# Optimization experiments

Hardware: AMD Instinct MI355X
Metric: run time of the kernel (lower is better)

The kernel has to match this reference:

```python
import jax, jax.numpy as jnp
import numpy as np

E = 16        # num_experts
TOPK = 2      # num_experts_per_tok


def setup_inputs() -> dict:
    key = jax.random.key(0)
    ks = jax.random.split(key, 8)
    B, S, H, I, IS = 4, 2048, 1024, 512, 2048
    std = 0.02
    return {
        "hidden_states": jax.random.normal(ks[0], (B, S, H), jnp.float32),
        "gate_w": jax.random.normal(ks[1], (E, H), jnp.float32) * std,
        "gate_up_proj": jax.random.normal(ks[2], (E, 2 * I, H), jnp.float32) * std,
        "down_proj": jax.random.normal(ks[3], (E, H, I), jnp.float32) * std,
        "shared_gate_proj": jax.random.normal(ks[4], (IS, H), jnp.float32) * std,
        "shared_up_proj": jax.random.normal(ks[5], (IS, H), jnp.float32) * std,
        "shared_down_proj": jax.random.normal(ks[6], (H, IS), jnp.float32) * std,
        "shared_expert_gate_w": jax.random.normal(ks[7], (1, H), jnp.float32) * std,
    }


def _moe(x, gate_w, gate_up_proj, down_proj, sgp, sup, sdp, segw):
    # x: [N, H] flattened tokens
    N = x.shape[0]
    router_logits = x @ gate_w.T                      # [N, E]
    probs = jax.nn.softmax(router_logits, axis=-1)
    routing_weights, selected = jax.lax.top_k(probs, TOPK)   # [N, TOPK]
    routing_weights = routing_weights / routing_weights.sum(-1, keepdims=True)
    # combine weights scattered into dense [N, E] (per-token per-expert gate)
    combine = jnp.zeros((N, E), x.dtype).at[jnp.arange(N)[:, None], selected].add(routing_weights)

    def body(acc, ws):
        gu_w, d_w, cw = ws                            # [2I,H], [H,I], [N]
        gu = x @ gu_w.T                               # [N, 2I]
        g, u = jnp.split(gu, 2, axis=-1)
        h = jax.nn.silu(g) * u                        # [N, I]
        return acc + cw[:, None] * (h @ d_w.T), None

    expert_out, _ = jax.lax.scan(body, jnp.zeros_like(x), (gate_up_proj, down_proj, combine.T))

    # shared expert with sigmoid token gate
    shared_h = jax.nn.silu(x @ sgp.T) * (x @ sup.T)   # [N, IS]
    shared_out = (shared_h @ sdp.T) * jax.nn.sigmoid(x @ segw.T)  # [N, H]
    out = expert_out + shared_out

    # aux (load-balancing) loss
    counts = jnp.sum(jax.nn.one_hot(selected, E, dtype=x.dtype), axis=(0, 1))  # [E]
    frac_tokens = counts / (N * TOPK)
    frac_probs = probs.sum(0) / N
    aux_loss = E * jnp.sum(frac_tokens * frac_probs)
    return out, aux_loss


def reference(hidden_states, gate_w, gate_up_proj, down_proj, shared_gate_proj, shared_up_proj, shared_down_proj, shared_expert_gate_w):
    B, S, H = hidden_states.shape
    out, aux = _moe(hidden_states.reshape(-1, H), gate_w, gate_up_proj, down_proj,
                    shared_gate_proj, shared_up_proj, shared_down_proj, shared_expert_gate_w)
    return out.reshape(B, S, H), aux
```

## Files before the change

### kernel.cpp

```cpp
#include <hip/hip_runtime.h>
#include <hip/hip_bf16.h>
#include <stdint.h>


#define N_TOK 8192
#define HDIM 1024
#define NEXP 16
#define IEXP 512
#define ISH 2048

typedef __bf16 bf16x8 __attribute__((ext_vector_type(8)));
typedef float f32x4 __attribute__((ext_vector_type(4)));

#define OFF_XBF   ((size_t)0)
#define OFF_WSG   ((size_t)16777216)
#define OFF_WSU   ((size_t)20971520)
#define OFF_WSD   ((size_t)25165824)
#define OFF_SH    ((size_t)29360128)
#define OFF_HEXP  ((size_t)62914560)
#define OFF_IDS   ((size_t)79691776)
#define OFF_META  ((size_t)80216064)
#define OFF_SIG   ((size_t)80216320)
#define OFF_LG    ((size_t)80249088)
#define OFF_SLOT  ((size_t)81297664)
#define OFF_TWAB  ((size_t)81363200)

static __device__ __forceinline__ unsigned short f2bf(float f) {
  unsigned int u = __float_as_uint(f);
  u += 0x7fffu + ((u >> 16) & 1u);
  return (unsigned short)(u >> 16);
}
static __device__ __forceinline__ int pack_bf2(float a, float b) {
  return (int)f2bf(a) | ((int)f2bf(b) << 16);
}
static __device__ __forceinline__ float bf2f(unsigned short u) {
  return __uint_as_float(((unsigned int)u) << 16);
}
static __device__ __forceinline__ void gl_lds16(const void* g, void* l) {
  __builtin_amdgcn_global_load_lds(
      (const __attribute__((address_space(1))) unsigned int*)g,
      (__attribute__((address_space(3))) unsigned int*)l, 16, 0, 0);
}

__global__ void cvt_kernel(const float* __restrict__ src,
                           unsigned short* __restrict__ dst, int n4) {
  int i = blockIdx.x * 256 + threadIdx.x;
  if (i >= n4) return;
  float4 v = ((const float4*)src)[i];
  uint2 o;
  o.x = (unsigned)pack_bf2(v.x, v.y);
  o.y = (unsigned)pack_bf2(v.z, v.w);
  ((uint2*)dst)[i] = o;
}

__global__ __launch_bounds__(256) void logits_kernel(
    const float* __restrict__ X, const float* __restrict__ GW,
    const float* __restrict__ SEGW, float* __restrict__ LG,
    unsigned short* __restrict__ XBF) {
  int wid = threadIdx.x >> 6, lane = threadIdx.x & 63;
  int tok = blockIdx.x * 4 + wid;
  const float* xr = X + (size_t)tok * HDIM;
  unsigned short* xw = XBF + (size_t)tok * HDIM;
  float xv[16];
#pragma unroll
  for (int i = 0; i < 16; i++) xv[i] = xr[lane + 64 * i];
#pragma unroll
  for (int i = 0; i < 16; i++) xw[lane + 64 * i] = f2bf(xv[i]);
  float myv = 0.f;
#pragma unroll
  for (int e = 0; e < 17; e++) {
    const float* wr = (e < 16) ? (GW + (size_t)e * HDIM) : SEGW;
    float p = 0.f;
#pragma unroll
    for (int i = 0; i < 16; i++) p += xv[i] * wr[lane + 64 * i];
#pragma unroll
    for (int off = 32; off >= 1; off >>= 1) p += __shfl_xor(p, off, 64);
    if (lane == e) myv = p;
  }
  if (lane < 17) LG[(size_t)tok * 32 + lane] = myv;
}

__global__ __launch_bounds__(256) void route_kernel(
    const float* __restrict__ LG, int* __restrict__ cnt,
    float* __restrict__ pps, int* __restrict__ ids,
    int* __restrict__ slotAB, float* __restrict__ twAB,
    float* __restrict__ sig) {
  __shared__ int lcnt[16];
  __shared__ int lbase[16];
  __shared__ float lps[16];
  int tid = threadIdx.x;
  int tok = blockIdx.x * 256 + tid;
  if (tid < 16) { lcnt[tid] = 0; lps[tid] = 0.f; }
  __syncthreads();
  const float4* row = (const float4*)(LG + (size_t)tok * 32);
  float4 v0 = row[0], v1 = row[1], v2 = row[2], v3 = row[3];
  float g16 = row[4].x;
  float lg[16] = {v0.x, v0.y, v0.z, v0.w, v1.x, v1.y, v1.z, v1.w,
                  v2.x, v2.y, v2.z, v2.w, v3.x, v3.y, v3.z, v3.w};
  float mx = lg[0];
#pragma unroll
  for (int e = 1; e < 16; e++) mx = fmaxf(mx, lg[e]);
  float pr[16], s = 0.f;
#pragma unroll
  for (int e = 0; e < 16; e++) { pr[e] = __expf(lg[e] - mx); s += pr[e]; }
  float inv_s = 1.f / s;
  float p1 = -1.f, p2 = -1.f; int i1 = 0, i2 = 0;
#pragma unroll
  for (int e = 0; e < 16; e++) {
    if (pr[e] > p1) { p2 = p1; i2 = i1; p1 = pr[e]; i1 = e; }
    else if (pr[e] > p2) { p2 = pr[e]; i2 = e; }
  }
  float wsum = p1 + p2;
  int s1 = atomicAdd(&lcnt[i1], 1);
  int s2 = atomicAdd(&lcnt[i2], 1);
#pragma unroll
  for (int e = 0; e < 16; e++) atomicAdd(&lps[e], pr[e] * inv_s);
  sig[tok] = 1.f / (1.f + __expf(-g16));
  __syncthreads();
  if (tid < 16) {
    lbase[tid] = atomicAdd(&cnt[tid], lcnt[tid]);
    atomicAdd(&pps[tid], lps[tid]);
  }
  __syncthreads();
  int sl1 = lbase[i1] + s1, sl2 = lbase[i2] + s2;
  ids[i1 * N_TOK + sl1] = tok;
  ids[i2 * N_TOK + sl2] = tok;
  slotAB[tok * 2]     = (i1 << 14) | sl1;
  slotAB[tok * 2 + 1] = (i2 << 14) | sl2;
  twAB[tok * 2]     = p1 / wsum;
  twAB[tok * 2 + 1] = p2 / wsum;
}

__global__ void offs_aux_kernel(const int* __restrict__ cnt, int* __restrict__ off,
                                const float* __restrict__ probs_sum,
                                float* __restrict__ out_aux) {
  if (threadIdx.x == 0 && blockIdx.x == 0) {
    int run = 0; float aux = 0.f;
    for (int e = 0; e < NEXP; e++) {
      off[e] = run; run += cnt[e];
      aux += ((float)cnt[e] / (float)(N_TOK * 2)) * (probs_sum[e] / (float)N_TOK);
    }
    off[16] = run;
    *out_aux = (float)NEXP * aux;
  }
}

template <int MODE>
__global__ __launch_bounds__(512, 2) void gemm8p_kernel(
    const unsigned short* __restrict__ A,
    const unsigned short* __restrict__ B1,
    const unsigned short* __restrict__ B2,
    const int* __restrict__ ids, const int* __restrict__ cnt,
    const int* __restrict__ off, unsigned short* __restrict__ Out) {
  constexpr int KD = (MODE == 2) ? IEXP : HDIM;
  constexpr int NK = KD / 64;
  extern __shared__ unsigned short lds[];

  int ne, base, e;
  if constexpr (MODE == 0) { e = 0; ne = N_TOK; base = 0; }
  else { e = blockIdx.z; ne = cnt[e]; base = off[e]; }

  const int t = threadIdx.x, lane = t & 63, w = t >> 6;
  const int fr = lane & 15, hi = lane >> 4;
  const int rq = hi * 4;
  const int Rm = (w >> 2) * 64;
  const int wn = (w & 3) * 32;
  const int srow = t >> 3;
  const int sblk = t & 7;
  const int cb = (sblk ^ (srow & 7)) * 8;
  const int s0 = ((0 + hi) ^ (fr & 7)) * 8;
  const int s1 = ((4 + hi) ^ (fr & 7)) * 8;
  const f32x4 z = {0.f, 0.f, 0.f, 0.f};

#define STG_A(buf, h, kt)                                                     \
  do {                                                                        \
    gl_lds16(apt[h][0] + (kt) * 64, &lds[(buf)*32768 + (h)*8192 + t * 8]);    \
    gl_lds16(apt[h][1] + (kt) * 64,                                           \
             &lds[(buf)*32768 + (h)*8192 + 4096 + t * 8]);                    \
  } while (0)
#define STG_B(buf, h, kt)                                                     \
  do {                                                                        \
    gl_lds16(bpt[h][0] + (kt) * 64,                                           \
             &lds[(buf)*32768 + 16384 + (h)*8192 + t * 8]);                   \
    gl_lds16(bpt[h][1] + (kt) * 64,                                           \
             &lds[(buf)*32768 + 16384 + (h)*8192 + 4096 + t * 8]);            \
  } while (0)

  for (int m0 = blockIdx.y * 256; m0 < ne; m0 += gridDim.y * 256) {
    const unsigned short* apt[2][2];
    const unsigned short* bpt[2][2];
#pragma unroll
    for (int h = 0; h < 2; h++)
#pragma unroll
      for (int l = 0; l < 2; l++) {
        int r = h * 128 + l * 64 + srow;
        int arow;
        if constexpr (MODE == 0) {
          arow = m0 + r;
        } else if constexpr (MODE == 1) {
          int slot = m0 + r;
          arow = (slot < ne) ? ids[e * N_TOK + slot] : 0;
        } else {
          int ra = base + m0 + r;
          if (ra > 16383) ra = 16383;
          arow = ra;
        }
        apt[h][l] = A + (size_t)arow * KD + cb;
        if constexpr (MODE == 0) {
          int gcol = blockIdx.x * 128 + ((r >> 5) << 4) + (r & 15);
          const unsigned short* W = (r & 16) ? B2 : B1;
          bpt[h][l] = W + (size_t)gcol * HDIM + cb;
        } else if constexpr (MODE == 1) {
          int wrow = ((r & 16) ? 512 : 0) + blockIdx.x * 128 + ((r >> 5) << 4) + (r & 15);
          bpt[h][l] = B1 + ((size_t)e * 1024 + wrow) * HDIM + cb;
        } else {
          int nrow = blockIdx.x * 256 + r;
          bpt[h][l] = B1 + ((size_t)e * HDIM + nrow) * IEXP + cb;
        }
      }

    f32x4 acc[8][4];
#pragma unroll
    for (int i = 0; i < 8; i++)
#pragma unroll
      for (int j = 0; j < 4; j++) acc[i][j] = z;

    STG_A(0, 0, 0); STG_B(0, 1, 0); STG_A(0, 1, 0); STG_B(0, 0, 0);
    if (NK > 1) {
      STG_A(1, 0, 1); STG_B(1, 1, 1);
      asm volatile("s_waitcnt vmcnt(4)" ::: "memory");
    } else {
      asm volatile("s_waitcnt vmcnt(0)" ::: "memory");
    }
    __builtin_amdgcn_s_barrier();

    for (int kt = 0; kt < NK; ++kt) {
      const int c = kt & 1, nb = c ^ 1;
      const unsigned short* Ab = &lds[c * 32768];
      const unsigned short* Bb = &lds[c * 32768 + 16384];
      bf16x8 a[4][2], b[2][2];

#pragma unroll
      for (int i = 0; i < 4; i++) {
        int ro = (Rm + i * 16 + fr) * 64;
        a[i][0] = *(const bf16x8*)&Ab[ro + s0];
        a[i][1] = *(const bf16x8*)&Ab[ro + s1];
      }
#pragma unroll
      for (int j = 0; j < 2; j++) {
        int ro = (wn + j * 16 + fr) * 64;
        b[j][0] = *(const bf16x8*)&Bb[ro + s0];
        b[j][1] = *(const bf16x8*)&Bb[ro + s1];
      }
      if (kt + 1 < NK) STG_A(nb, 1, kt + 1);
      __builtin_amdgcn_s_barrier();
      asm volatile("s_waitcnt lgkmcnt(0)" ::: "memory");
      __builtin_amdgcn_s_setprio(1);
#pragma unroll
      for (int i = 0; i < 4; i++)
#pragma unroll
        for (int j = 0; j < 2; j++) {
          acc[i][j] = __builtin_amdgcn_mfma_f32_16x16x32_bf16(a[i][0], b[j][0], acc[i][j], 0, 0, 0);
          acc[i][j] = __builtin_amdgcn_mfma_f32_16x16x32_bf16(a[i][1], b[j][1], acc[i][j], 0, 0, 0);
        }
      __builtin_amdgcn_s_setprio(0);
      __builtin_amdgcn_s_barrier();

#pragma unroll
      for (int j = 0; j < 2; j++) {
        int ro = (128 + wn + j * 16 + fr) * 64;
        b[j][0] = *(const bf16x8*)&Bb[ro + s0];
        b[j][1] = *(const bf16x8*)&Bb[ro + s1];
      }
      if (kt + 1 < NK) STG_B(nb, 0, kt + 1);
      __builtin_amdgcn_s_barrier();
      asm volatile("s_waitcnt lgkmcnt(0)" ::: "memory");
      __builtin_amdgcn_s_setprio(1);
#pragma unroll
      for (int i = 0; i < 4; i++)
#pragma unroll
        for (int j = 0; j < 2; j++) {
          acc[i][2 + j] = __builtin_amdgcn_mfma_f32_16x16x32_bf16(a[i][0], b[j][0], acc[i][2 + j], 0, 0, 0);
          acc[i][2 + j] = __builtin_amdgcn_mfma_f32_16x16x32_bf16(a[i][1], b[j][1], acc[i][2 + j], 0, 0, 0);
        }
      __builtin_amdgcn_s_setprio(0);
      __builtin_amdgcn_s_barrier();

#pragma unroll
      for (int i = 0; i < 4; i++) {
        int ro = (128 + Rm + i * 16 + fr) * 64;
        a[i][0] = *(const bf16x8*)&Ab[ro + s0];
        a[i][1] = *(const bf16x8*)&Ab[ro + s1];
      }
      if (kt + 2 < NK) STG_A(c, 0, kt + 2);
      __builtin_amdgcn_s_barrier();
      asm volatile("s_waitcnt lgkmcnt(0)" ::: "memory");
      __builtin_amdgcn_s_setprio(1);
#pragma unroll
      for (int i = 0; i < 4; i++)
#pragma unroll
        for (int j = 0; j < 2; j++) {
          acc[4 + i][2 + j] = __builtin_amdgcn_mfma_f32_16x16x32_bf16(a[i][0], b[j][0], acc[4 + i][2 + j], 0, 0, 0);
          acc[4 + i][2 + j] = __builtin_amdgcn_mfma_f32_16x16x32_bf16(a[i][1], b[j][1], acc[4 + i][2 + j], 0, 0, 0);
        }
      __builtin_amdgcn_s_setprio(0);
      __builtin_amdgcn_s_barrier();

#pragma unroll
      for (int j = 0; j < 2; j++) {
        int ro = (wn + j * 16 + fr) * 64;
        b[j][0] = *(const bf16x8*)&Bb[ro + s0];
        b[j][1] = *(const bf16x8*)&Bb[ro + s1];
      }
      if (kt + 2 < NK) STG_B(c, 1, kt + 2);
      __builtin_amdgcn_s_barrier();
      asm volatile("s_waitcnt lgkmcnt(0)" ::: "memory");
      __builtin_amdgcn_s_setprio(1);
#pragma unroll
      for (int i = 0; i < 4; i++)
#pragma unroll
        for (int j = 0; j < 2; j++) {
          acc[4 + i][j] = __builtin_amdgcn_mfma_f32_16x16x32_bf16(a[i][0], b[j][0], acc[4 + i][j], 0, 0, 0);
          acc[4 + i][j] = __builtin_amdgcn_mfma_f32_16x16x32_bf16(a[i][1], b[j][1], acc[4 + i][j], 0, 0, 0);
        }
      __builtin_amdgcn_s_setprio(0);
      if (kt + 2 < NK) asm volatile("s_waitcnt vmcnt(4)" ::: "memory");
      else             asm volatile("s_waitcnt vmcnt(0)" ::: "memory");
      __builtin_amdgcn_s_barrier();
    }

#pragma unroll
    for (int i = 0; i < 8; i++) {
      int mloc = (i >> 2) * 128 + Rm + (i & 3) * 16 + rq;
      if constexpr (MODE == 2) {
#pragma unroll
        for (int j = 0; j < 4; j++) {
          int nn = blockIdx.x * 256 + (j >> 1) * 128 + wn + (j & 1) * 16 + fr;
#pragma unroll
          for (int r = 0; r < 4; r++) {
            int slot = m0 + mloc + r;
            if (slot < ne)
              Out[(size_t)(base + slot) * HDIM + nn] = f2bf(acc[i][j][r]);
          }
        }
      } else {
#pragma unroll
        for (int p = 0; p < 2; p++) {
          int cc = blockIdx.x * 128 + p * 64 + (w & 3) * 16 + fr;
#pragma unroll
          for (int r = 0; r < 4; r++) {
            int slot = m0 + mloc + r;
            float g = acc[i][2 * p][r], u = acc[i][2 * p + 1][r];
            float hv = g / (1.f + __expf(-g)) * u;
            if constexpr (MODE == 0) {
              Out[(size_t)slot * ISH + cc] = f2bf(hv);
            } else {
              if (slot < ne)
                Out[(size_t)(base + slot) * IEXP + cc] = f2bf(hv);
            }
          }
        }
      }
    }
  }
#undef STG_A
#undef STG_B
}

__global__ __launch_bounds__(256) void shared_gemm2_kernel(
    const unsigned short* __restrict__ H, const unsigned short* __restrict__ Wd,
    const float* __restrict__ sig, float* __restrict__ Out) {
  __shared__ __align__(16) unsigned short As[128 * 32];
  __shared__ __align__(16) unsigned short Bs[128 * 32];
  int m0 = blockIdx.y * 128, n0 = blockIdx.x * 128;
  int t = threadIdx.x, lane = t & 63, w = t >> 6;
  int wm = (w & 1) * 64, wn = (w >> 1) * 64;
  int arow = t >> 2, akb = (t & 3) * 8;
  const unsigned short* apA0 = H + (size_t)(m0 + arow) * ISH + akb;
  const unsigned short* apA1 = H + (size_t)(m0 + 64 + arow) * ISH + akb;
  const unsigned short* apB0 = Wd + (size_t)(n0 + arow) * ISH + akb;
  const unsigned short* apB1 = Wd + (size_t)(n0 + 64 + arow) * ISH + akb;
  f32x4 z = {0.f, 0.f, 0.f, 0.f};
  f32x4 acc[4][4];
#pragma unroll
  for (int i = 0; i < 4; i++)
#pragma unroll
    for (int j = 0; j < 4; j++) acc[i][j] = z;
  for (int k0 = 0; k0 < ISH; k0 += 32) {
    __syncthreads();
    gl_lds16(apA0 + k0, &As[t * 8]);
    gl_lds16(apA1 + k0, &As[2048 + t * 8]);
    gl_lds16(apB0 + k0, &Bs[t * 8]);
    gl_lds16(apB1 + k0, &Bs[2048 + t * 8]);
    __syncthreads();
    int fr = lane & 15, fc = (lane >> 4) * 8;
    bf16x8 af[4], bfr[4];
#pragma unroll
    for (int i = 0; i < 4; i++) {
      af[i] = *(const bf16x8*)&As[(wm + i * 16 + fr) * 32 + fc];
      bfr[i] = *(const bf16x8*)&Bs[(wn + i * 16 + fr) * 32 + fc];
    }
#pragma unroll
    for (int i = 0; i < 4; i++)
#pragma unroll
      for (int j = 0; j < 4; j++)
        acc[i][j] = __builtin_amdgcn_mfma_f32_16x16x32_bf16(af[i], bfr[j], acc[i][j], 0, 0, 0);
  }
  int col = lane & 15, rq = (lane >> 4) * 4;
#pragma unroll
  for (int i = 0; i < 4; i++)
#pragma unroll
    for (int r = 0; r < 4; r++) {
      int mm = m0 + wm + i * 16 + rq + r;
      float sg = sig[mm];
#pragma unroll
      for (int j = 0; j < 4; j++) {
        int nn = n0 + wn + j * 16 + col;
        Out[(size_t)mm * HDIM + nn] = acc[i][j][r] * sg;
      }
    }
}

__global__ __launch_bounds__(256) void combine_kernel(
    const unsigned short* __restrict__ Eout, const int* __restrict__ slotAB,
    const float* __restrict__ twAB, const int* __restrict__ off,
    float* __restrict__ Out) {
  int tok = blockIdx.x, t = threadIdx.x;
  int sa = slotAB[tok * 2], sb = slotAB[tok * 2 + 1];
  float wa = twAB[tok * 2], wb = twAB[tok * 2 + 1];
  int ra = off[sa >> 14] + (sa & 16383);
  int rb = off[sb >> 14] + (sb & 16383);
  const ushort4 a4 = *(const ushort4*)(Eout + (size_t)ra * HDIM + t * 4);
  const ushort4 b4 = *(const ushort4*)(Eout + (size_t)rb * HDIM + t * 4);
  float* po = Out + (size_t)tok * HDIM + t * 4;
  float4 o = *(const float4*)po;
  o.x += wa * bf2f(a4.x) + wb * bf2f(b4.x);
  o.y += wa * bf2f(a4.y) + wb * bf2f(b4.y);
  o.z += wa * bf2f(a4.z) + wb * bf2f(b4.z);
  o.w += wa * bf2f(a4.w) + wb * bf2f(b4.w);
  *(float4*)po = o;
}

extern "C" void kernel_launch(void* const* d_in, const int* in_sizes, int n_in,
                              void* d_out, int out_size, void* d_ws, size_t ws_size,
                              hipStream_t stream) {
  const float* X   = (const float*)d_in[0];
  const float* GW  = (const float*)d_in[1];
  const float* WGU = (const float*)d_in[2];
  const float* WDN = (const float*)d_in[3];
  const float* WSG = (const float*)d_in[4];
  const float* WSU = (const float*)d_in[5];
  const float* WSD = (const float*)d_in[6];
  const float* SEGW = (const float*)d_in[7];
  float* Out = (float*)d_out;
  char* ws = (char*)d_ws;

  unsigned short* xbf  = (unsigned short*)(ws + OFF_XBF);
  unsigned short* wsg  = (unsigned short*)(ws + OFF_WSG);
  unsigned short* wsu  = (unsigned short*)(ws + OFF_WSU);
  unsigned short* wsd  = (unsigned short*)(ws + OFF_WSD);
  unsigned short* sh   = (unsigned short*)(ws + OFF_SH);
  unsigned short* hexp = (unsigned short*)(ws + OFF_HEXP);
  int*   ids  = (int*)(ws + OFF_IDS);
  int*   cnt  = (int*)(ws + OFF_META);
  int*   off  = (int*)(ws + OFF_META + 64);
  float* pps  = (float*)(ws + OFF_META + 144);
  float* sig  = (float*)(ws + OFF_SIG);
  float* lg   = (float*)(ws + OFF_LG);
  int*   slotAB = (int*)(ws + OFF_SLOT);
  float* twAB   = (float*)(ws + OFF_TWAB);
  unsigned short* wgu_bf = (unsigned short*)(ws + OFF_SH);
  unsigned short* wdn_bf = (unsigned short*)(ws + OFF_XBF);
  unsigned short* eout   = (unsigned short*)(ws + OFF_SH);

  (void)hipFuncSetAttribute((const void*)gemm8p_kernel<0>,
                            hipFuncAttributeMaxDynamicSharedMemorySize, 131072);
  (void)hipFuncSetAttribute((const void*)gemm8p_kernel<1>,
                            hipFuncAttributeMaxDynamicSharedMemorySize, 131072);
  (void)hipFuncSetAttribute((const void*)gemm8p_kernel<2>,
                            hipFuncAttributeMaxDynamicSharedMemorySize, 131072);

  hipMemsetAsync(ws + OFF_META, 0, 256, stream);

  {
    int n4;
    n4 = (ISH * HDIM) / 4;
    cvt_kernel<<<(n4 + 255) / 256, 256, 0, stream>>>(WSG, wsg, n4);
    cvt_kernel<<<(n4 + 255) / 256, 256, 0, stream>>>(WSU, wsu, n4);
    n4 = (HDIM * ISH) / 4;
    cvt_kernel<<<(n4 + 255) / 256, 256, 0, stream>>>(WSD, wsd, n4);
  }

  logits_kernel<<<N_TOK / 4, 256, 0, stream>>>(X, GW, SEGW, lg, xbf);
  route_kernel<<<N_TOK / 256, 256, 0, stream>>>(lg, cnt, pps, ids, slotAB, twAB, sig);
  offs_aux_kernel<<<1, 64, 0, stream>>>(cnt, off, pps, Out + (size_t)N_TOK * HDIM);

  gemm8p_kernel<0><<<dim3(ISH * 2 / 256, N_TOK / 256), 512, 131072, stream>>>(
      xbf, wsg, wsu, ids, cnt, off, sh);
  shared_gemm2_kernel<<<dim3(HDIM / 128, N_TOK / 128), 256, 0, stream>>>(sh, wsd, sig, Out);

  {
    int n4 = (NEXP * 2 * IEXP * HDIM) / 4;
    cvt_kernel<<<(n4 + 255) / 256, 256, 0, stream>>>(WGU, wgu_bf, n4);
  }
  gemm8p_kernel<1><<<dim3(IEXP * 2 / 256, 8, NEXP), 512, 131072, stream>>>(
      xbf, wgu_bf, wgu_bf, ids, cnt, off, hexp);
  {
    int n4 = (NEXP * HDIM * IEXP) / 4;
    cvt_kernel<<<(n4 + 255) / 256, 256, 0, stream>>>(WDN, wdn_bf, n4);
  }
  gemm8p_kernel<2><<<dim3(HDIM / 256, 8, NEXP), 512, 131072, stream>>>(
      hexp, wdn_bf, wdn_bf, ids, cnt, off, eout);
  combine_kernel<<<N_TOK, 256, 0, stream>>>(eout, slotAB, twAB, off, Out);
}
```

Baseline: 507.7 us.

## Merge shared down-proj with expert gate-up GEMM and fuse combine via atomics

Replaces the separate shared-expert down-projection kernel and combine kernel with a unified GEMM template. One launch covers both the routed-expert gate/up GEMM and a split-K shared down-projection, so the two run concurrently. The expert down-projection now scatters weighted results into a zeroed fp32 output with atomicAdd, which removes the bf16 intermediate and the combine pass. It also drops the per-phase lgkmcnt waits and extra barriers in the inner loop, and relocates the expert weight conversions when the workspace is large enough. In exchange it adds atomic traffic, a full output memset, and nondeterministic summation order.

```diff
diff --git a/kernel.cpp b/kernel.cpp
--- a/kernel.cpp
+++ b/kernel.cpp
@@ -25,6 +25,10 @@
 #define OFF_SLOT  ((size_t)81297664)
 #define OFF_TWAB  ((size_t)81363200)
 
+#define WGU_NEW   ((size_t)81428736)
+#define WDN_NEW   ((size_t)(WGU_NEW + 33554432))
+#define NEED_MERGED ((size_t)(WDN_NEW + 16777216))
+
 static __device__ __forceinline__ unsigned short f2bf(float f) {
   unsigned int u = __float_as_uint(f);
   u += 0x7fffu + ((u >> 16) & 1u);
@@ -33,13 +37,15 @@
 static __device__ __forceinline__ int pack_bf2(float a, float b) {
   return (int)f2bf(a) | ((int)f2bf(b) << 16);
 }
-static __device__ __forceinline__ float bf2f(unsigned short u) {
-  return __uint_as_float(((unsigned int)u) << 16);
-}
 static __device__ __forceinline__ void gl_lds16(const void* g, void* l) {
   __builtin_amdgcn_global_load_lds(
       (const __attribute__((address_space(1))) unsigned int*)g,
       (__attribute__((address_space(3))) unsigned int*)l, 16, 0, 0);
+}
+static __device__ __forceinline__ void barf() {
+  asm volatile("" ::: "memory");
+  __builtin_amdgcn_s_barrier();
+  asm volatile("" ::: "memory");
 }
 
 __global__ void cvt_kernel(const float* __restrict__ src,
@@ -145,20 +151,45 @@
   }
 }
 
-template <int MODE>
-__global__ __launch_bounds__(512, 2) void gemm8p_kernel(
-    const unsigned short* __restrict__ A,
+__global__ __launch_bounds__(256) void tws_kernel(
+    const int* __restrict__ slotAB, const float* __restrict__ twAB,
+    const int* __restrict__ off, float* __restrict__ tws) {
+  int tok = blockIdx.x * 256 + threadIdx.x;
+  int sa = slotAB[tok * 2], sb = slotAB[tok * 2 + 1];
+  tws[off[sa >> 14] + (sa & 16383)] = twAB[tok * 2];
+  tws[off[sb >> 14] + (sb & 16383)] = twAB[tok * 2 + 1];
+}
+
+template <int TMODE>
+__global__ __launch_bounds__(512, 2) void g8p_kernel(
+    const unsigned short* __restrict__ A0,
+    const unsigned short* __restrict__ A1,
     const unsigned short* __restrict__ B1,
     const unsigned short* __restrict__ B2,
+    const unsigned short* __restrict__ B3,
     const int* __restrict__ ids, const int* __restrict__ cnt,
-    const int* __restrict__ off, unsigned short* __restrict__ Out) {
-  constexpr int KD = (MODE == 2) ? IEXP : HDIM;
-  constexpr int NK = KD / 64;
+    const int* __restrict__ off, const float* __restrict__ tws,
+    const float* __restrict__ sig,
+    unsigned short* __restrict__ OBf, float* __restrict__ OF, int zoff) {
   extern __shared__ unsigned short lds[];
 
-  int ne, base, e;
-  if constexpr (MODE == 0) { e = 0; ne = N_TOK; base = 0; }
-  else { e = blockIdx.z; ne = cnt[e]; base = off[e]; }
+  int rmode, e = 0, kls = 0, mt = 0;
+  if constexpr (TMODE == 13) {
+    int z = blockIdx.z + zoff;
+    if (z < 16) { rmode = 1; e = z; }
+    else { rmode = 3; int zp = z - 16; mt = (zp >> 2) * 8 + blockIdx.y; kls = zp & 3; }
+  } else if constexpr (TMODE == 2) {
+    rmode = 2; e = blockIdx.z >> 1; kls = blockIdx.z & 1;
+  } else {
+    rmode = 0;
+  }
+
+  int ne, base = 0;
+  if (rmode == 1 || rmode == 2) { ne = cnt[e]; base = off[e]; }
+  else ne = N_TOK;
+
+  const int NK = (TMODE == 0) ? 16 : (TMODE == 2) ? 4 : (rmode == 1 ? 16 : 8);
+  const int kofs = (rmode == 2) ? kls * 256 : (rmode == 3) ? kls * 512 : 0;
 
   const int t = threadIdx.x, lane = t & 63, w = t >> 6;
   const int fr = lane & 15, hi = lane >> 4;
@@ -170,7 +201,11 @@
   const int cb = (sblk ^ (srow & 7)) * 8;
   const int s0 = ((0 + hi) ^ (fr & 7)) * 8;
   const int s1 = ((4 + hi) ^ (fr & 7)) * 8;
-  const f32x4 z = {0.f, 0.f, 0.f, 0.f};
+  const f32x4 z4 = {0.f, 0.f, 0.f, 0.f};
+
+  int m0start, m0end, m0step;
+  if (rmode == 3) { m0start = mt * 256; m0end = m0start + 256; m0step = 8192; }
+  else { m0start = blockIdx.y * 256; m0end = ne; m0step = (int)gridDim.y * 256; }
 
 #define STG_A(buf, h, kt)                                                     \
   do {                                                                        \
@@ -186,7 +221,7 @@
              &lds[(buf)*32768 + 16384 + (h)*8192 + 4096 + t * 8]);            \
   } while (0)
 
-  for (int m0 = blockIdx.y * 256; m0 < ne; m0 += gridDim.y * 256) {
+  for (int m0 = m0start; m0 < m0end; m0 += m0step) {
     const unsigned short* apt[2][2];
     const unsigned short* bpt[2][2];
 #pragma unroll
@@ -194,28 +229,32 @@
 #pragma unroll
       for (int l = 0; l < 2; l++) {
         int r = h * 128 + l * 64 + srow;
-        int arow;
-        if constexpr (MODE == 0) {
-          arow = m0 + r;
-        } else if constexpr (MODE == 1) {
+        if (rmode == 0) {
+          apt[h][l] = A0 + (size_t)(m0 + r) * HDIM + cb;
+        } else if (rmode == 1) {
           int slot = m0 + r;
-          arow = (slot < ne) ? ids[e * N_TOK + slot] : 0;
-        } else {
+          int arow = (slot < ne) ? ids[e * N_TOK + slot] : 0;
+          apt[h][l] = A0 + (size_t)arow * HDIM + cb;
+        } else if (rmode == 2) {
           int ra = base + m0 + r;
           if (ra > 16383) ra = 16383;
-          arow = ra;
-        }
-        apt[h][l] = A + (size_t)arow * KD + cb;
-        if constexpr (MODE == 0) {
+          apt[h][l] = A0 + (size_t)ra * IEXP + kofs + cb;
+        } else {
+          apt[h][l] = A1 + (size_t)(m0 + r) * ISH + kofs + cb;
+        }
+        if (rmode == 0) {
           int gcol = blockIdx.x * 128 + ((r >> 5) << 4) + (r & 15);
           const unsigned short* W = (r & 16) ? B2 : B1;
           bpt[h][l] = W + (size_t)gcol * HDIM + cb;
-        } else if constexpr (MODE == 1) {
+        } else if (rmode == 1) {
           int wrow = ((r & 16) ? 512 : 0) + blockIdx.x * 128 + ((r >> 5) << 4) + (r & 15);
           bpt[h][l] = B1 + ((size_t)e * 1024 + wrow) * HDIM + cb;
+        } else if (rmode == 2) {
+          int nrow = blockIdx.x * 256 + r;
+          bpt[h][l] = B1 + ((size_t)e * HDIM + nrow) * IEXP + kofs + cb;
         } else {
           int nrow = blockIdx.x * 256 + r;
-          bpt[h][l] = B1 + ((size_t)e * HDIM + nrow) * IEXP + cb;
+          bpt[h][l] = B3 + (size_t)nrow * ISH + kofs + cb;
         }
       }
 
@@ -223,16 +262,12 @@
 #pragma unroll
     for (int i = 0; i < 8; i++)
 #pragma unroll
-      for (int j = 0; j < 4; j++) acc[i][j] = z;
+      for (int j = 0; j < 4; j++) acc[i][j] = z4;
 
     STG_A(0, 0, 0); STG_B(0, 1, 0); STG_A(0, 1, 0); STG_B(0, 0, 0);
-    if (NK > 1) {
-      STG_A(1, 0, 1); STG_B(1, 1, 1);
-      asm volatile("s_waitcnt vmcnt(4)" ::: "memory");
-    } else {
-      asm volatile("s_waitcnt vmcnt(0)" ::: "memory");
-    }
-    __builtin_amdgcn_s_barrier();
+    STG_A(1, 0, 1); STG_B(1, 1, 1);
+    asm volatile("s_waitcnt vmcnt(4)" ::: "memory");
+    barf();
 
     for (int kt = 0; kt < NK; ++kt) {
       const int c = kt & 1, nb = c ^ 1;
@@ -253,8 +288,6 @@
         b[j][1] = *(const bf16x8*)&Bb[ro + s1];
       }
       if (kt + 1 < NK) STG_A(nb, 1, kt + 1);
-      __builtin_amdgcn_s_barrier();
-      asm volatile("s_waitcnt lgkmcnt(0)" ::: "memory");
       __builtin_amdgcn_s_setprio(1);
 #pragma unroll
       for (int i = 0; i < 4; i++)
@@ -264,7 +297,7 @@
           acc[i][j] = __builtin_amdgcn_mfma_f32_16x16x32_bf16(a[i][1], b[j][1], acc[i][j], 0, 0, 0);
         }
       __builtin_amdgcn_s_setprio(0);
-      __builtin_amdgcn_s_barrier();
+      barf();
 
 #pragma unroll
       for (int j = 0; j < 2; j++) {
@@ -273,8 +306,6 @@
         b[j][1] = *(const bf16x8*)&Bb[ro + s1];
       }
       if (kt + 1 < NK) STG_B(nb, 0, kt + 1);
-      __builtin_amdgcn_s_barrier();
-      asm volatile("s_waitcnt lgkmcnt(0)" ::: "memory");
       __builtin_amdgcn_s_setprio(1);
 #pragma unroll
       for (int i = 0; i < 4; i++)
@@ -284,7 +315,7 @@
           acc[i][2 + j] = __builtin_amdgcn_mfma_f32_16x16x32_bf16(a[i][1], b[j][1], acc[i][2 + j], 0, 0, 0);
         }
       __builtin_amdgcn_s_setprio(0);
-      __builtin_amdgcn_s_barrier();
+      barf();
 
 #pragma unroll
       for (int i = 0; i < 4; i++) {
@@ -293,8 +324,6 @@
         a[i][1] = *(const bf16x8*)&Ab[ro + s1];
       }
       if (kt + 2 < NK) STG_A(c, 0, kt + 2);
-      __builtin_amdgcn_s_barrier();
-      asm volatile("s_waitcnt lgkmcnt(0)" ::: "memory");
       __builtin_amdgcn_s_setprio(1);
 #pragma unroll
       for (int i = 0; i < 4; i++)
@@ -304,7 +333,7 @@
           acc[4 + i][2 + j] = __builtin_amdgcn_mfma_f32_16x16x32_bf16(a[i][1], b[j][1], acc[4 + i][2 + j], 0, 0, 0);
         }
       __builtin_amdgcn_s_setprio(0);
-      __builtin_amdgcn_s_barrier();
+      barf();
 
 #pragma unroll
       for (int j = 0; j < 2; j++) {
@@ -313,8 +342,6 @@
         b[j][1] = *(const bf16x8*)&Bb[ro + s1];
       }
       if (kt + 2 < NK) STG_B(c, 1, kt + 2);
-      __builtin_amdgcn_s_barrier();
-      asm volatile("s_waitcnt lgkmcnt(0)" ::: "memory");
       __builtin_amdgcn_s_setprio(1);
 #pragma unroll
       for (int i = 0; i < 4; i++)
@@ -326,24 +353,13 @@
       __builtin_amdgcn_s_setprio(0);
       if (kt + 2 < NK) asm volatile("s_waitcnt vmcnt(4)" ::: "memory");
       else             asm volatile("s_waitcnt vmcnt(0)" ::: "memory");
-      __builtin_amdgcn_s_barrier();
+      barf();
     }
 
 #pragma unroll
     for (int i = 0; i < 8; i++) {
       int mloc = (i >> 2) * 128 + Rm + (i & 3) * 16 + rq;
-      if constexpr (MODE == 2) {
-#pragma unroll
-        for (int j = 0; j < 4; j++) {
-          int nn = blockIdx.x * 256 + (j >> 1) * 128 + wn + (j & 1) * 16 + fr;
-#pragma unroll
-          for (int r = 0; r < 4; r++) {
-            int slot = m0 + mloc + r;
-            if (slot < ne)
-              Out[(size_t)(base + slot) * HDIM + nn] = f2bf(acc[i][j][r]);
-          }
-        }
-      } else {
+      if (rmode == 0 || rmode == 1) {
 #pragma unroll
         for (int p = 0; p < 2; p++) {
           int cc = blockIdx.x * 128 + p * 64 + (w & 3) * 16 + fr;
@@ -352,93 +368,43 @@
             int slot = m0 + mloc + r;
             float g = acc[i][2 * p][r], u = acc[i][2 * p + 1][r];
             float hv = g / (1.f + __expf(-g)) * u;
-            if constexpr (MODE == 0) {
-              Out[(size_t)slot * ISH + cc] = f2bf(hv);
-            } else {
-              if (slot < ne)
-                Out[(size_t)(base + slot) * IEXP + cc] = f2bf(hv);
+            if (rmode == 0) {
+              OBf[(size_t)slot * ISH + cc] = f2bf(hv);
+            } else if (slot < ne) {
+              OBf[(size_t)(base + slot) * IEXP + cc] = f2bf(hv);
             }
           }
         }
+      } else if (rmode == 2) {
+#pragma unroll
+        for (int r = 0; r < 4; r++) {
+          int slot = m0 + mloc + r;
+          if (slot < ne) {
+            int tok = ids[e * N_TOK + slot];
+            float tw = tws[base + slot];
+#pragma unroll
+            for (int j = 0; j < 4; j++) {
+              int nn = blockIdx.x * 256 + (j >> 1) * 128 + wn + (j & 1) * 16 + fr;
+              atomicAdd(&OF[(size_t)tok * HDIM + nn], tw * acc[i][j][r]);
+            }
+          }
+        }
+      } else {
+#pragma unroll
+        for (int r = 0; r < 4; r++) {
+          int m = m0 + mloc + r;
+          float sv = sig[m];
+#pragma unroll
+          for (int j = 0; j < 4; j++) {
+            int nn = blockIdx.x * 256 + (j >> 1) * 128 + wn + (j & 1) * 16 + fr;
+            atomicAdd(&OF[(size_t)m * HDIM + nn], sv * acc[i][j][r]);
+          }
+        }
       }
     }
   }
 #undef STG_A
 #undef STG_B
-}
-
-__global__ __launch_bounds__(256) void shared_gemm2_kernel(
-    const unsigned short* __restrict__ H, const unsigned short* __restrict__ Wd,
-    const float* __restrict__ sig, float* __restrict__ Out) {
-  __shared__ __align__(16) unsigned short As[128 * 32];
-  __shared__ __align__(16) unsigned short Bs[128 * 32];
-  int m0 = blockIdx.y * 128, n0 = blockIdx.x * 128;
-  int t = threadIdx.x, lane = t & 63, w = t >> 6;
-  int wm = (w & 1) * 64, wn = (w >> 1) * 64;
-  int arow = t >> 2, akb = (t & 3) * 8;
-  const unsigned short* apA0 = H + (size_t)(m0 + arow) * ISH + akb;
-  const unsigned short* apA1 = H + (size_t)(m0 + 64 + arow) * ISH + akb;
-  const unsigned short* apB0 = Wd + (size_t)(n0 + arow) * ISH + akb;
-  const unsigned short* apB1 = Wd + (size_t)(n0 + 64 + arow) * ISH + akb;
-  f32x4 z = {0.f, 0.f, 0.f, 0.f};
-  f32x4 acc[4][4];
-#pragma unroll
-  for (int i = 0; i < 4; i++)
-#pragma unroll
-    for (int j = 0; j < 4; j++) acc[i][j] = z;
-  for (int k0 = 0; k0 < ISH; k0 += 32) {
-    __syncthreads();
-    gl_lds16(apA0 + k0, &As[t * 8]);
-    gl_lds16(apA1 + k0, &As[2048 + t * 8]);
-    gl_lds16(apB0 + k0, &Bs[t * 8]);
-    gl_lds16(apB1 + k0, &Bs[2048 + t * 8]);
-    __syncthreads();
-    int fr = lane & 15, fc = (lane >> 4) * 8;
-    bf16x8 af[4], bfr[4];
-#pragma unroll
-    for (int i = 0; i < 4; i++) {
-      af[i] = *(const bf16x8*)&As[(wm + i * 16 + fr) * 32 + fc];
-      bfr[i] = *(const bf16x8*)&Bs[(wn + i * 16 + fr) * 32 + fc];
-    }
-#pragma unroll
-    for (int i = 0; i < 4; i++)
-#pragma unroll
-      for (int j = 0; j < 4; j++)
-        acc[i][j] = __builtin_amdgcn_mfma_f32_16x16x32_bf16(af[i], bfr[j], acc[i][j], 0, 0, 0);
-  }
-  int col = lane & 15, rq = (lane >> 4) * 4;
-#pragma unroll
-  for (int i = 0; i < 4; i++)
-#pragma unroll
-    for (int r = 0; r < 4; r++) {
-      int mm = m0 + wm + i * 16 + rq + r;
-      float sg = sig[mm];
-#pragma unroll
-      for (int j = 0; j < 4; j++) {
-        int nn = n0 + wn + j * 16 + col;
-        Out[(size_t)mm * HDIM + nn] = acc[i][j][r] * sg;
-      }
-    }
-}
-
-__global__ __launch_bounds__(256) void combine_kernel(
-    const unsigned short* __restrict__ Eout, const int* __restrict__ slotAB,
-    const float* __restrict__ twAB, const int* __restrict__ off,
-    float* __restrict__ Out) {
-  int tok = blockIdx.x, t = threadIdx.x;
-  int sa = slotAB[tok * 2], sb = slotAB[tok * 2 + 1];
-  float wa = twAB[tok * 2], wb = twAB[tok * 2 + 1];
-  int ra = off[sa >> 14] + (sa & 16383);
-  int rb = off[sb >> 14] + (sb & 16383);
-  const ushort4 a4 = *(const ushort4*)(Eout + (size_t)ra * HDIM + t * 4);
-  const ushort4 b4 = *(const ushort4*)(Eout + (size_t)rb * HDIM + t * 4);
-  float* po = Out + (size_t)tok * HDIM + t * 4;
-  float4 o = *(const float4*)po;
-  o.x += wa * bf2f(a4.x) + wb * bf2f(b4.x);
-  o.y += wa * bf2f(a4.y) + wb * bf2f(b4.y);
-  o.z += wa * bf2f(a4.z) + wb * bf2f(b4.z);
-  o.w += wa * bf2f(a4.w) + wb * bf2f(b4.w);
-  *(float4*)po = o;
 }
 
 extern "C" void kernel_launch(void* const* d_in, const int* in_sizes, int n_in,
@@ -467,20 +433,23 @@
   float* pps  = (float*)(ws + OFF_META + 144);
   float* sig  = (float*)(ws + OFF_SIG);
   float* lg   = (float*)(ws + OFF_LG);
+  float* tws  = (float*)(ws + OFF_LG);
   int*   slotAB = (int*)(ws + OFF_SLOT);
   float* twAB   = (float*)(ws + OFF_TWAB);
-  unsigned short* wgu_bf = (unsigned short*)(ws + OFF_SH);
-  unsigned short* wdn_bf = (unsigned short*)(ws + OFF_XBF);
-  unsigned short* eout   = (unsigned short*)(ws + OFF_SH);
-
-  (void)hipFuncSetAttribute((const void*)gemm8p_kernel<0>,
+
+  const bool merged = (ws_size >= NEED_MERGED);
+  unsigned short* wgu_bf = (unsigned short*)(ws + (merged ? WGU_NEW : OFF_SH));
+  unsigned short* wdn_bf = (unsigned short*)(ws + (merged ? WDN_NEW : OFF_XBF));
+
+  (void)hipFuncSetAttribute((const void*)g8p_kernel<0>,
                             hipFuncAttributeMaxDynamicSharedMemorySize, 131072);
-  (void)hipFuncSetAttribute((const void*)gemm8p_kernel<1>,
+  (void)hipFuncSetAttribute((const void*)g8p_kernel<2>,
                             hipFuncAttributeMaxDynamicSharedMemorySize, 131072);
-  (void)hipFuncSetAttribute((const void*)gemm8p_kernel<2>,
+  (void)hipFuncSetAttribute((const void*)g8p_kernel<13>,
                             hipFuncAttributeMaxDynamicSharedMemorySize, 131072);
 
   hipMemsetAsync(ws + OFF_META, 0, 256, stream);
+  hipMemsetAsync(Out, 0, (size_t)N_TOK * HDIM * 4, stream);
 
   {
     int n4;
@@ -490,26 +459,39 @@
     n4 = (HDIM * ISH) / 4;
     cvt_kernel<<<(n4 + 255) / 256, 256, 0, stream>>>(WSD, wsd, n4);
   }
+  if (merged) {
+    int n4 = (NEXP * 2 * IEXP * HDIM) / 4;
+    cvt_kernel<<<(n4 + 255) / 256, 256, 0, stream>>>(WGU, wgu_bf, n4);
+    n4 = (NEXP * HDIM * IEXP) / 4;
+    cvt_kernel<<<(n4 + 255) / 256, 256, 0, stream>>>(WDN, wdn_bf, n4);
+  }
 
   logits_kernel<<<N_TOK / 4, 256, 0, stream>>>(X, GW, SEGW, lg, xbf);
   route_kernel<<<N_TOK / 256, 256, 0, stream>>>(lg, cnt, pps, ids, slotAB, twAB, sig);
   offs_aux_kernel<<<1, 64, 0, stream>>>(cnt, off, pps, Out + (size_t)N_TOK * HDIM);
-
-  gemm8p_kernel<0><<<dim3(ISH * 2 / 256, N_TOK / 256), 512, 131072, stream>>>(
-      xbf, wsg, wsu, ids, cnt, off, sh);
-  shared_gemm2_kernel<<<dim3(HDIM / 128, N_TOK / 128), 256, 0, stream>>>(sh, wsd, sig, Out);
-
-  {
-    int n4 = (NEXP * 2 * IEXP * HDIM) / 4;
-    cvt_kernel<<<(n4 + 255) / 256, 256, 0, stream>>>(WGU, wgu_bf, n4);
-  }
-  gemm8p_kernel<1><<<dim3(IEXP * 2 / 256, 8, NEXP), 512, 131072, stream>>>(
-      xbf, wgu_bf, wgu_bf, ids, cnt, off, hexp);
-  {
-    int n4 = (NEXP * HDIM * IEXP) / 4;
-    cvt_kernel<<<(n4 + 255) / 256, 256, 0, stream>>>(WDN, wdn_bf, n4);
-  }
-  gemm8p_kernel<2><<<dim3(HDIM / 256, 8, NEXP), 512, 131072, stream>>>(
-      hexp, wdn_bf, wdn_bf, ids, cnt, off, eout);
-  combine_kernel<<<N_TOK, 256, 0, stream>>>(eout, slotAB, twAB, off, Out);
-}
+  tws_kernel<<<N_TOK / 256, 256, 0, stream>>>(slotAB, twAB, off, tws);
+
+  g8p_kernel<0><<<dim3(ISH * 2 / 256, N_TOK / 256, 1), 512, 131072, stream>>>(
+      xbf, nullptr, wsg, wsu, nullptr, ids, cnt, off, tws, sig, sh, Out, 0);
+
+  if (merged) {
+    g8p_kernel<13><<<dim3(4, 8, 32), 512, 131072, stream>>>(
+        xbf, sh, wgu_bf, nullptr, wsd, ids, cnt, off, tws, sig, hexp, Out, 0);
+  } else {
+    g8p_kernel<13><<<dim3(4, 8, 16), 512, 131072, stream>>>(
+        xbf, sh, wgu_bf, nullptr, wsd, ids, cnt, off, tws, sig, hexp, Out, 16);
+    {
+      int n4 = (NEXP * 2 * IEXP * HDIM) / 4;
+      cvt_kernel<<<(n4 + 255) / 256, 256, 0, stream>>>(WGU, wgu_bf, n4);
+    }
+    g8p_kernel<13><<<dim3(4, 8, 16), 512, 131072, stream>>>(
+        xbf, sh, wgu_bf, nullptr, wsd, ids, cnt, off, tws, sig, hexp, Out, 0);
+    {
+      int n4 = (NEXP * HDIM * IEXP) / 4;
+      cvt_kernel<<<(n4 + 255) / 256, 256, 0, stream>>>(WDN, wdn_bf, n4);
+    }
+  }
+
+  g8p_kernel<2><<<dim3(4, 8, 32), 512, 131072, stream>>>(
+      hexp, nullptr, wdn_bf, nullptr, nullptr, ids, cnt, off, tws, sig, nullptr, Out, 0);
+}
```

Result: slower. 674.3 us (+32.8%).

## Merge shared gate-up and expert gate-up GEMMs into one launch, drop per-phase waits

Applied to the files above, without the earlier changes.

Adds a combined GEMM mode that runs the shared-expert gate/up GEMM and the routed-expert gate/up GEMM in a single 1024-block launch. Block IDs are decoded into either role, and the expert weight conversion moves earlier into a separate workspace region when the workspace is large enough. The aim is to fill the GPU better and cut launch and tail gaps between the two GEMMs. It also removes the intra-iteration barriers and lgkmcnt waits after LDS reads, which risks relying on compiler-inserted waits for correctness. It adds runtime mode branching inside the kernel.

```diff
diff --git a/kernel.cpp b/kernel.cpp
--- a/kernel.cpp
+++ b/kernel.cpp
@@ -25,6 +25,9 @@
 #define OFF_SLOT  ((size_t)81297664)
 #define OFF_TWAB  ((size_t)81363200)
 
+#define WGU_NEW     ((size_t)81428736)
+#define NEED_MERGED ((size_t)(WGU_NEW + 33554432))
+
 static __device__ __forceinline__ unsigned short f2bf(float f) {
   unsigned int u = __float_as_uint(f);
   u += 0x7fffu + ((u >> 16) & 1u);
@@ -40,6 +43,11 @@
   __builtin_amdgcn_global_load_lds(
       (const __attribute__((address_space(1))) unsigned int*)g,
       (__attribute__((address_space(3))) unsigned int*)l, 16, 0, 0);
+}
+static __device__ __forceinline__ void barf() {
+  asm volatile("" ::: "memory");
+  __builtin_amdgcn_s_barrier();
+  asm volatile("" ::: "memory");
 }
 
 __global__ void cvt_kernel(const float* __restrict__ src,
@@ -145,20 +153,43 @@
   }
 }
 
-template <int MODE>
-__global__ __launch_bounds__(512, 2) void gemm8p_kernel(
-    const unsigned short* __restrict__ A,
-    const unsigned short* __restrict__ B1,
-    const unsigned short* __restrict__ B2,
+template <int TMODE>
+__global__ __launch_bounds__(512, 2) void g8p_kernel(
+    const unsigned short* __restrict__ A0,
+    const unsigned short* __restrict__ Bg,
+    const unsigned short* __restrict__ Bu,
+    const unsigned short* __restrict__ Bgu,
+    const unsigned short* __restrict__ Bd,
     const int* __restrict__ ids, const int* __restrict__ cnt,
-    const int* __restrict__ off, unsigned short* __restrict__ Out) {
-  constexpr int KD = (MODE == 2) ? IEXP : HDIM;
+    const int* __restrict__ off,
+    unsigned short* __restrict__ Osh,
+    unsigned short* __restrict__ Ohex,
+    unsigned short* __restrict__ Oeout) {
+  constexpr int KD = (TMODE == 2) ? IEXP : HDIM;
   constexpr int NK = KD / 64;
   extern __shared__ unsigned short lds[];
 
-  int ne, base, e;
-  if constexpr (MODE == 0) { e = 0; ne = N_TOK; base = 0; }
-  else { e = blockIdx.z; ne = cnt[e]; base = off[e]; }
+  int rmode, e = 0, bx, by, m0step;
+  if constexpr (TMODE == 3) {
+    int id = blockIdx.x;
+    if (id < 512) { rmode = 0; bx = id & 15; by = id >> 4; m0step = 8192; }
+    else {
+      int id2 = id - 512;
+      rmode = 1; e = id2 >> 5; bx = id2 & 3; by = (id2 >> 2) & 7; m0step = 2048;
+    }
+  } else if constexpr (TMODE == 0) {
+    rmode = 0; bx = blockIdx.x; by = blockIdx.y; m0step = 8192;
+  } else if constexpr (TMODE == 1) {
+    rmode = 1; e = blockIdx.z; bx = blockIdx.x; by = blockIdx.y;
+    m0step = (int)gridDim.y * 256;
+  } else {
+    rmode = 2; e = blockIdx.z; bx = blockIdx.x; by = blockIdx.y;
+    m0step = (int)gridDim.y * 256;
+  }
+
+  int ne, base = 0;
+  if (rmode == 0) { ne = N_TOK; }
+  else { ne = cnt[e]; base = off[e]; }
 
   const int t = threadIdx.x, lane = t & 63, w = t >> 6;
   const int fr = lane & 15, hi = lane >> 4;
@@ -170,7 +201,7 @@
   const int cb = (sblk ^ (srow & 7)) * 8;
   const int s0 = ((0 + hi) ^ (fr & 7)) * 8;
   const int s1 = ((4 + hi) ^ (fr & 7)) * 8;
-  const f32x4 z = {0.f, 0.f, 0.f, 0.f};
+  const f32x4 z4 = {0.f, 0.f, 0.f, 0.f};
 
 #define STG_A(buf, h, kt)                                                     \
   do {                                                                        \
@@ -186,7 +217,7 @@
              &lds[(buf)*32768 + 16384 + (h)*8192 + 4096 + t * 8]);            \
   } while (0)
 
-  for (int m0 = blockIdx.y * 256; m0 < ne; m0 += gridDim.y * 256) {
+  for (int m0 = by * 256; m0 < ne; m0 += m0step) {
     const unsigned short* apt[2][2];
     const unsigned short* bpt[2][2];
 #pragma unroll
@@ -194,28 +225,27 @@
 #pragma unroll
       for (int l = 0; l < 2; l++) {
         int r = h * 128 + l * 64 + srow;
-        int arow;
-        if constexpr (MODE == 0) {
-          arow = m0 + r;
-        } else if constexpr (MODE == 1) {
+        if (rmode == 0) {
+          apt[h][l] = A0 + (size_t)(m0 + r) * HDIM + cb;
+        } else if (rmode == 1) {
           int slot = m0 + r;
-          arow = (slot < ne) ? ids[e * N_TOK + slot] : 0;
+          int arow = (slot < ne) ? ids[e * N_TOK + slot] : 0;
+          apt[h][l] = A0 + (size_t)arow * HDIM + cb;
         } else {
           int ra = base + m0 + r;
           if (ra > 16383) ra = 16383;
-          arow = ra;
-        }
-        apt[h][l] = A + (size_t)arow * KD + cb;
-        if constexpr (MODE == 0) {
-          int gcol = blockIdx.x * 128 + ((r >> 5) << 4) + (r & 15);
-          const unsigned short* W = (r & 16) ? B2 : B1;
+          apt[h][l] = A0 + (size_t)ra * IEXP + cb;
+        }
+        if (rmode == 0) {
+          int gcol = bx * 128 + ((r >> 5) << 4) + (r & 15);
+          const unsigned short* W = (r & 16) ? Bu : Bg;
           bpt[h][l] = W + (size_t)gcol * HDIM + cb;
-        } else if constexpr (MODE == 1) {
-          int wrow = ((r & 16) ? 512 : 0) + blockIdx.x * 128 + ((r >> 5) << 4) + (r & 15);
-          bpt[h][l] = B1 + ((size_t)e * 1024 + wrow) * HDIM + cb;
+        } else if (rmode == 1) {
+          int wrow = ((r & 16) ? 512 : 0) + bx * 128 + ((r >> 5) << 4) + (r & 15);
+          bpt[h][l] = Bgu + ((size_t)e * 1024 + wrow) * HDIM + cb;
         } else {
-          int nrow = blockIdx.x * 256 + r;
-          bpt[h][l] = B1 + ((size_t)e * HDIM + nrow) * IEXP + cb;
+          int nrow = bx * 256 + r;
+          bpt[h][l] = Bd + ((size_t)e * HDIM + nrow) * IEXP + cb;
         }
       }
 
@@ -223,16 +253,12 @@
 #pragma unroll
     for (int i = 0; i < 8; i++)
 #pragma unroll
-      for (int j = 0; j < 4; j++) acc[i][j] = z;
+      for (int j = 0; j < 4; j++) acc[i][j] = z4;
 
     STG_A(0, 0, 0); STG_B(0, 1, 0); STG_A(0, 1, 0); STG_B(0, 0, 0);
-    if (NK > 1) {
-      STG_A(1, 0, 1); STG_B(1, 1, 1);
-      asm volatile("s_waitcnt vmcnt(4)" ::: "memory");
-    } else {
-      asm volatile("s_waitcnt vmcnt(0)" ::: "memory");
-    }
-    __builtin_amdgcn_s_barrier();
+    STG_A(1, 0, 1); STG_B(1, 1, 1);
+    asm volatile("s_waitcnt vmcnt(4)" ::: "memory");
+    barf();
 
     for (int kt = 0; kt < NK; ++kt) {
       const int c = kt & 1, nb = c ^ 1;
@@ -253,8 +279,6 @@
         b[j][1] = *(const bf16x8*)&Bb[ro + s1];
       }
       if (kt + 1 < NK) STG_A(nb, 1, kt + 1);
-      __builtin_amdgcn_s_barrier();
-      asm volatile("s_waitcnt lgkmcnt(0)" ::: "memory");
       __builtin_amdgcn_s_setprio(1);
 #pragma unroll
       for (int i = 0; i < 4; i++)
@@ -264,7 +288,7 @@
           acc[i][j] = __builtin_amdgcn_mfma_f32_16x16x32_bf16(a[i][1], b[j][1], acc[i][j], 0, 0, 0);
         }
       __builtin_amdgcn_s_setprio(0);
-      __builtin_amdgcn_s_barrier();
+      barf();
 
 #pragma unroll
       for (int j = 0; j < 2; j++) {
@@ -273,8 +297,6 @@
         b[j][1] = *(const bf16x8*)&Bb[ro + s1];
       }
       if (kt + 1 < NK) STG_B(nb, 0, kt + 1);
-      __builtin_amdgcn_s_barrier();
-      asm volatile("s_waitcnt lgkmcnt(0)" ::: "memory");
       __builtin_amdgcn_s_setprio(1);
 #pragma unroll
       for (int i = 0; i < 4; i++)
@@ -284,7 +306,7 @@
           acc[i][2 + j] = __builtin_amdgcn_mfma_f32_16x16x32_bf16(a[i][1], b[j][1], acc[i][2 + j], 0, 0, 0);
         }
       __builtin_amdgcn_s_setprio(0);
-      __builtin_amdgcn_s_barrier();
+      barf();
 
 #pragma unroll
       for (int i = 0; i < 4; i++) {
@@ -293,8 +315,6 @@
         a[i][1] = *(const bf16x8*)&Ab[ro + s1];
       }
       if (kt + 2 < NK) STG_A(c, 0, kt + 2);
-      __builtin_amdgcn_s_barrier();
-      asm volatile("s_waitcnt lgkmcnt(0)" ::: "memory");
       __builtin_amdgcn_s_setprio(1);
 #pragma unroll
       for (int i = 0; i < 4; i++)
@@ -304,7 +324,7 @@
           acc[4 + i][2 + j] = __builtin_amdgcn_mfma_f32_16x16x32_bf16(a[i][1], b[j][1], acc[4 + i][2 + j], 0, 0, 0);
         }
       __builtin_amdgcn_s_setprio(0);
-      __builtin_amdgcn_s_barrier();
+      barf();
 
 #pragma unroll
       for (int j = 0; j < 2; j++) {
@@ -313,8 +333,6 @@
         b[j][1] = *(const bf16x8*)&Bb[ro + s1];
       }
       if (kt + 2 < NK) STG_B(c, 1, kt + 2);
-      __builtin_amdgcn_s_barrier();
-      asm volatile("s_waitcnt lgkmcnt(0)" ::: "memory");
       __builtin_amdgcn_s_setprio(1);
 #pragma unroll
       for (int i = 0; i < 4; i++)
@@ -326,37 +344,36 @@
       __builtin_amdgcn_s_setprio(0);
       if (kt + 2 < NK) asm volatile("s_waitcnt vmcnt(4)" ::: "memory");
       else             asm volatile("s_waitcnt vmcnt(0)" ::: "memory");
-      __builtin_amdgcn_s_barrier();
+      barf();
     }
 
 #pragma unroll
     for (int i = 0; i < 8; i++) {
       int mloc = (i >> 2) * 128 + Rm + (i & 3) * 16 + rq;
-      if constexpr (MODE == 2) {
+      if (rmode == 2) {
 #pragma unroll
         for (int j = 0; j < 4; j++) {
-          int nn = blockIdx.x * 256 + (j >> 1) * 128 + wn + (j & 1) * 16 + fr;
+          int nn = bx * 256 + (j >> 1) * 128 + wn + (j & 1) * 16 + fr;
 #pragma unroll
           for (int r = 0; r < 4; r++) {
             int slot = m0 + mloc + r;
             if (slot < ne)
-              Out[(size_t)(base + slot) * HDIM + nn] = f2bf(acc[i][j][r]);
+              Oeout[(size_t)(base + slot) * HDIM + nn] = f2bf(acc[i][j][r]);
           }
         }
       } else {
 #pragma unroll
         for (int p = 0; p < 2; p++) {
-          int cc = blockIdx.x * 128 + p * 64 + (w & 3) * 16 + fr;
+          int cc = bx * 128 + p * 64 + (w & 3) * 16 + fr;
 #pragma unroll
           for (int r = 0; r < 4; r++) {
             int slot = m0 + mloc + r;
             float g = acc[i][2 * p][r], u = acc[i][2 * p + 1][r];
             float hv = g / (1.f + __expf(-g)) * u;
-            if constexpr (MODE == 0) {
-              Out[(size_t)slot * ISH + cc] = f2bf(hv);
-            } else {
-              if (slot < ne)
-                Out[(size_t)(base + slot) * IEXP + cc] = f2bf(hv);
+            if (rmode == 0) {
+              Osh[(size_t)slot * ISH + cc] = f2bf(hv);
+            } else if (slot < ne) {
+              Ohex[(size_t)(base + slot) * IEXP + cc] = f2bf(hv);
             }
           }
         }
@@ -469,15 +486,19 @@
   float* lg   = (float*)(ws + OFF_LG);
   int*   slotAB = (int*)(ws + OFF_SLOT);
   float* twAB   = (float*)(ws + OFF_TWAB);
-  unsigned short* wgu_bf = (unsigned short*)(ws + OFF_SH);
+
+  const bool merged = (ws_size >= NEED_MERGED);
+  unsigned short* wgu_bf = (unsigned short*)(ws + (merged ? WGU_NEW : OFF_SH));
   unsigned short* wdn_bf = (unsigned short*)(ws + OFF_XBF);
   unsigned short* eout   = (unsigned short*)(ws + OFF_SH);
 
-  (void)hipFuncSetAttribute((const void*)gemm8p_kernel<0>,
+  (void)hipFuncSetAttribute((const void*)g8p_kernel<0>,
                             hipFuncAttributeMaxDynamicSharedMemorySize, 131072);
-  (void)hipFuncSetAttribute((const void*)gemm8p_kernel<1>,
+  (void)hipFuncSetAttribute((const void*)g8p_kernel<1>,
                             hipFuncAttributeMaxDynamicSharedMemorySize, 131072);
-  (void)hipFuncSetAttribute((const void*)gemm8p_kernel<2>,
+  (void)hipFuncSetAttribute((const void*)g8p_kernel<2>,
+                            hipFuncAttributeMaxDynamicSharedMemorySize, 131072);
+  (void)hipFuncSetAttribute((const void*)g8p_kernel<3>,
                             hipFuncAttributeMaxDynamicSharedMemorySize, 131072);
 
   hipMemsetAsync(ws + OFF_META, 0, 256, stream);
@@ -490,26 +511,36 @@
     n4 = (HDIM * ISH) / 4;
     cvt_kernel<<<(n4 + 255) / 256, 256, 0, stream>>>(WSD, wsd, n4);
   }
+  if (merged) {
+    int n4 = (NEXP * 2 * IEXP * HDIM) / 4;
+    cvt_kernel<<<(n4 + 255) / 256, 256, 0, stream>>>(WGU, wgu_bf, n4);
+  }
 
   logits_kernel<<<N_TOK / 4, 256, 0, stream>>>(X, GW, SEGW, lg, xbf);
   route_kernel<<<N_TOK / 256, 256, 0, stream>>>(lg, cnt, pps, ids, slotAB, twAB, sig);
   offs_aux_kernel<<<1, 64, 0, stream>>>(cnt, off, pps, Out + (size_t)N_TOK * HDIM);
 
-  gemm8p_kernel<0><<<dim3(ISH * 2 / 256, N_TOK / 256), 512, 131072, stream>>>(
-      xbf, wsg, wsu, ids, cnt, off, sh);
-  shared_gemm2_kernel<<<dim3(HDIM / 128, N_TOK / 128), 256, 0, stream>>>(sh, wsd, sig, Out);
-
-  {
-    int n4 = (NEXP * 2 * IEXP * HDIM) / 4;
-    cvt_kernel<<<(n4 + 255) / 256, 256, 0, stream>>>(WGU, wgu_bf, n4);
-  }
-  gemm8p_kernel<1><<<dim3(IEXP * 2 / 256, 8, NEXP), 512, 131072, stream>>>(
-      xbf, wgu_bf, wgu_bf, ids, cnt, off, hexp);
+  if (merged) {
+    g8p_kernel<3><<<dim3(1024), 512, 131072, stream>>>(
+        xbf, wsg, wsu, wgu_bf, nullptr, ids, cnt, off, sh, hexp, nullptr);
+    shared_gemm2_kernel<<<dim3(HDIM / 128, N_TOK / 128), 256, 0, stream>>>(sh, wsd, sig, Out);
+  } else {
+    g8p_kernel<0><<<dim3(16, 32), 512, 131072, stream>>>(
+        xbf, wsg, wsu, nullptr, nullptr, ids, cnt, off, sh, nullptr, nullptr);
+    shared_gemm2_kernel<<<dim3(HDIM / 128, N_TOK / 128), 256, 0, stream>>>(sh, wsd, sig, Out);
+    {
+      int n4 = (NEXP * 2 * IEXP * HDIM) / 4;
+      cvt_kernel<<<(n4 + 255) / 256, 256, 0, stream>>>(WGU, wgu_bf, n4);
+    }
+    g8p_kernel<1><<<dim3(4, 8, NEXP), 512, 131072, stream>>>(
+        xbf, nullptr, nullptr, wgu_bf, nullptr, ids, cnt, off, nullptr, hexp, nullptr);
+  }
+
   {
     int n4 = (NEXP * HDIM * IEXP) / 4;
     cvt_kernel<<<(n4 + 255) / 256, 256, 0, stream>>>(WDN, wdn_bf, n4);
   }
-  gemm8p_kernel<2><<<dim3(HDIM / 256, 8, NEXP), 512, 131072, stream>>>(
-      hexp, wdn_bf, wdn_bf, ids, cnt, off, eout);
+  g8p_kernel<2><<<dim3(HDIM / 256, 8, NEXP), 512, 131072, stream>>>(
+      hexp, nullptr, nullptr, nullptr, wdn_bf, ids, cnt, off, nullptr, nullptr, eout);
   combine_kernel<<<N_TOK, 256, 0, stream>>>(eout, slotAB, twAB, off, Out);
 }
```

Result: no change. 509.8 us (+0.4%).
